# Kernel tuning notes

Measured on AMD Instinct MI355X. Metric: run time of the kernel, lower is better.

## Reference

```python
import jax, jax.numpy as jnp
import numpy as np

B_BATCH, H_DIM, W_DIM, D_MODEL, N_STATE = 4, 64, 64, 512, 8


def setup_inputs() -> dict:
    key = jax.random.key(0)
    ks = jax.random.split(key, 7)
    x = jax.random.normal(ks[0], (B_BATCH, H_DIM * W_DIM, D_MODEL), jnp.float32)
    # stable diagonal recurrence: 0 < A < 1
    A = jax.random.uniform(ks[1], (D_MODEL, N_STATE), jnp.float32, 0.5, 0.99)
    Bm = jax.random.normal(ks[2], (D_MODEL, N_STATE), jnp.float32) * 0.1
    Cm = jax.random.normal(ks[3], (D_MODEL, N_STATE), jnp.float32) * 0.1
    D_skip = jax.random.normal(ks[4], (D_MODEL,), jnp.float32)
    Wp = jax.random.normal(ks[5], (D_MODEL, D_MODEL), jnp.float32) / np.sqrt(D_MODEL)
    b_proj = jnp.zeros((D_MODEL,), jnp.float32)
    return {"x": x, "h": H_DIM, "w": W_DIM, "A": A, "Bm": Bm, "Cm": Cm,
            "D_skip": D_skip, "Wp": Wp, "b_proj": b_proj}


def _ssm(xs, A, Bm, Cm, D_skip):
    # xs: (batch', L, d). Diagonal SSM: s_t = A*s_{t-1} + B*x_t; y_t = C.s_t + D*x_t
    bt, L, d = xs.shape
    n = A.shape[1]

    def step(s, x_t):  # s: (bt, d, n), x_t: (bt, d)
        s = A * s + Bm * x_t[:, :, None]
        y = jnp.einsum('bdn,dn->bd', s, Cm) + D_skip * x_t
        return s, y

    s0 = jnp.zeros((bt, d, n), xs.dtype)
    _, ys = jax.lax.scan(step, s0, jnp.swapaxes(xs, 0, 1))  # ys: (L, bt, d)
    return jnp.swapaxes(ys, 0, 1)


def reference(x, h, w, A, Bm, Cm, D_skip, Wp, b_proj):
    b, l, d = x.shape
    xg = x.reshape(b, h, w, d)
    # horizontal direction: 'b (h w) d -> (b w) h d' -> scan over h
    x_h = jnp.transpose(xg, (0, 2, 1, 3)).reshape(b * w, h, d)
    y_h = _ssm(x_h, A, Bm, Cm, D_skip).reshape(b, w, h, d)
    y_h = jnp.transpose(y_h, (0, 2, 1, 3)).reshape(b, l, d)
    # vertical direction: 'b (h w) d -> (b h) w d' -> scan over w
    x_v = xg.reshape(b * h, w, d)
    y_v = _ssm(x_v, A, Bm, Cm, D_skip).reshape(b, l, d)
    # fused add + output projection (Linear: x @ W.T + b)
    return (y_h + y_v) @ Wp.T + b_proj
```

## Files before the change

kernel.cpp:

```cpp
#include <hip/hip_runtime.h>

#define BB 4
#define HH 64
#define WW 64
#define DD 512
#define NS 8
#define MROWS (BB * HH * WW)

typedef __attribute__((ext_vector_type(8))) __bf16 bf16x8;
typedef __attribute__((ext_vector_type(4))) float f32x4;

__device__ inline short f2bf(float f) {
  unsigned u = __float_as_uint(f);
  return (short)((u + 0x7fff + ((u >> 16) & 1)) >> 16);
}
__device__ inline float bf2f(short s) {
  return __uint_as_float(((unsigned)(unsigned short)s) << 16);
}

template <bool HORIZ>
__global__ __launch_bounds__(256) void scan_kernel(
    const float* __restrict__ x, const float* __restrict__ A,
    const float* __restrict__ Bm, const float* __restrict__ Cm,
    const float* __restrict__ Dsk, short* __restrict__ y,
    const float* __restrict__ Wp, short* __restrict__ wb) {
  if (HORIZ && blockIdx.x >= 256) {
    const int cid = (blockIdx.x - 256) * 2 + blockIdx.y;
    const int i = (cid * 256 + (int)threadIdx.x) * 8;
    const float4 v0 = *(const float4*)&Wp[i];
    const float4 v1 = *(const float4*)&Wp[i + 4];
    short r[8];
    r[0] = f2bf(v0.x); r[1] = f2bf(v0.y); r[2] = f2bf(v0.z); r[3] = f2bf(v0.w);
    r[4] = f2bf(v1.x); r[5] = f2bf(v1.y); r[6] = f2bf(v1.z); r[7] = f2bf(v1.w);
    *(short4*)&wb[i] = *(short4*)&r[0];
    *(short4*)&wb[i + 4] = *(short4*)&r[4];
    return;
  }

  const int seq = blockIdx.x;
  const int d = blockIdx.y * 256 + threadIdx.x;
  const int b = seq >> 6;
  const int r = seq & 63;

  size_t base, step;
  if (HORIZ) {
    base = ((size_t)b * HH * WW + r) * DD + d;
    step = (size_t)WW * DD;
  } else {
    base = ((size_t)(b * HH + r)) * WW * DD + d;
    step = DD;
  }

  float a[NS], bm[NS], cm[NS], s[NS];
#pragma unroll
  for (int i = 0; i < NS; i += 4) {
    float4 t;
    t = *(const float4*)&A[(size_t)d * NS + i];
    a[i] = t.x; a[i + 1] = t.y; a[i + 2] = t.z; a[i + 3] = t.w;
    t = *(const float4*)&Bm[(size_t)d * NS + i];
    bm[i] = t.x; bm[i + 1] = t.y; bm[i + 2] = t.z; bm[i + 3] = t.w;
    t = *(const float4*)&Cm[(size_t)d * NS + i];
    cm[i] = t.x; cm[i + 1] = t.y; cm[i + 2] = t.z; cm[i + 3] = t.w;
  }
  const float dk = Dsk[d];
#pragma unroll
  for (int i = 0; i < NS; ++i) s[i] = 0.f;

  float xs[2][8];
  float yp[2][8];
#pragma unroll
  for (int i = 0; i < 8; ++i) xs[0][i] = x[base + (size_t)i * step];
  if (!HORIZ) {
#pragma unroll
    for (int i = 0; i < 8; ++i) yp[0][i] = bf2f(y[base + (size_t)i * step]);
  }

#pragma unroll 2
  for (int c = 0; c < 8; ++c) {
    const int cur = c & 1, nxt = cur ^ 1;
    const size_t nbase = base + 8 * step;
    if (c < 7) {
#pragma unroll
      for (int i = 0; i < 8; ++i) xs[nxt][i] = x[nbase + (size_t)i * step];
      if (!HORIZ) {
#pragma unroll
        for (int i = 0; i < 8; ++i)
          yp[nxt][i] = bf2f(y[nbase + (size_t)i * step]);
      }
    }
#pragma unroll
    for (int i = 0; i < 8; ++i) {
      const float xv = xs[cur][i];
      float acc = dk * xv;
#pragma unroll
      for (int n = 0; n < NS; ++n) {
        s[n] = fmaf(a[n], s[n], bm[n] * xv);
        acc = fmaf(s[n], cm[n], acc);
      }
      if (!HORIZ) acc += yp[cur][i];
      y[base + (size_t)i * step] = f2bf(acc);
    }
    base = nbase;
  }
}

#define GBM 128
#define GBN 128
#define GBK 64

__global__ __launch_bounds__(256) void gemm_bf16(
    const short* __restrict__ Y, const short* __restrict__ Wb,
    const float* __restrict__ bias, float* __restrict__ out) {
  __shared__ __align__(16) short As[GBM * GBK];
  __shared__ __align__(16) short Bs[GBN * GBK];

  const int tid = threadIdx.x;
  const int lane = tid & 63;
  const int wid = tid >> 6;
  const int wm = wid >> 1, wn = wid & 1;
  const int m0 = blockIdx.y * GBM;
  const int n0 = blockIdx.x * GBN;

  const int srow = lane >> 3;
  const int scol = (lane & 7) * 8;

  f32x4 acc[4][4];
#pragma unroll
  for (int m = 0; m < 4; ++m)
#pragma unroll
    for (int n = 0; n < 4; ++n) acc[m][n] = (f32x4){0.f, 0.f, 0.f, 0.f};

  auto stage = [&](int k0) {
#pragma unroll
    for (int c = 0; c < 4; ++c) {
      const int chunk = wid * 4 + c;
      const int row = chunk * 8 + srow;
      const short* ga = &Y[(size_t)(m0 + row) * DD + k0 + scol];
      const short* gb = &Wb[(size_t)(n0 + row) * DD + k0 + scol];
      __builtin_amdgcn_global_load_lds(
          (const __attribute__((address_space(1))) unsigned int*)ga,
          (__attribute__((address_space(3))) unsigned int*)((char*)As +
                                                            chunk * 1024),
          16, 0, 0);
      __builtin_amdgcn_global_load_lds(
          (const __attribute__((address_space(1))) unsigned int*)gb,
          (__attribute__((address_space(3))) unsigned int*)((char*)Bs +
                                                            chunk * 1024),
          16, 0, 0);
    }
  };

  const int arow = wm * 64 + (lane & 15);
  const int brow = wn * 64 + (lane & 15);
  const int kfr = (lane >> 4) * 8;

  stage(0);
  const int NK = DD / GBK;
  for (int k = 0; k < NK; ++k) {
    __syncthreads();
#pragma unroll
    for (int kk = 0; kk < GBK; kk += 32) {
      bf16x8 af[4], bfr[4];
      const int kcol = kk + kfr;
#pragma unroll
      for (int m = 0; m < 4; ++m)
        af[m] = *(const bf16x8*)(const void*)&As[(arow + m * 16) * GBK + kcol];
#pragma unroll
      for (int n = 0; n < 4; ++n)
        bfr[n] = *(const bf16x8*)(const void*)&Bs[(brow + n * 16) * GBK + kcol];
#pragma unroll
      for (int m = 0; m < 4; ++m)
#pragma unroll
        for (int n = 0; n < 4; ++n)
          acc[m][n] = __builtin_amdgcn_mfma_f32_16x16x32_bf16(
              af[m], bfr[n], acc[m][n], 0, 0, 0);
    }
    if (k + 1 < NK) {
      __syncthreads();
      stage((k + 1) * GBK);
    }
  }

  const int c16 = lane & 15;
  const int r4 = (lane >> 4) * 4;
#pragma unroll
  for (int m = 0; m < 4; ++m) {
    const int rowb = m0 + wm * 64 + m * 16 + r4;
#pragma unroll
    for (int n = 0; n < 4; ++n) {
      const int col = n0 + wn * 64 + n * 16 + c16;
      const float bv = bias[col];
#pragma unroll
      for (int j = 0; j < 4; ++j)
        out[(size_t)(rowb + j) * DD + col] = acc[m][n][j] + bv;
    }
  }
}

extern "C" void kernel_launch(void* const* d_in, const int* in_sizes, int n_in,
                              void* d_out, int out_size, void* d_ws,
                              size_t ws_size, hipStream_t stream) {
  const float* x = (const float*)d_in[0];
  const float* A = (const float*)d_in[3];
  const float* Bm = (const float*)d_in[4];
  const float* Cm = (const float*)d_in[5];
  const float* Dsk = (const float*)d_in[6];
  const float* Wp = (const float*)d_in[7];
  const float* bpj = (const float*)d_in[8];
  float* out = (float*)d_out;

  short* yws = (short*)d_ws;
  short* wb = (short*)((char*)d_ws + (size_t)MROWS * DD * 2);

  const dim3 grid_h(256 + 64, DD / 256);
  scan_kernel<true><<<grid_h, 256, 0, stream>>>(x, A, Bm, Cm, Dsk, yws, Wp, wb);
  const dim3 grid_v(256, DD / 256);
  scan_kernel<false><<<grid_v, 256, 0, stream>>>(x, A, Bm, Cm, Dsk, yws, Wp,
                                                 wb);

  const dim3 gemm_grid(DD / GBN, MROWS / GBM);
  gemm_bf16<<<gemm_grid, 256, 0, stream>>>(yws, wb, bpj, out);
}
```

Before: 48.21 us.

## Fuse vertical scan with output projection GEMM in one kernel

The vertical-direction scan now runs inside the GEMM kernel. Each 512-thread block scans one image row of 64 tokens across all 512 channels and writes the summed bf16 activations straight into swizzled LDS. It then multiplies them by the full 512-column weight matrix, staged in 64-wide K slices with XOR swizzling. This removes one kernel launch and the global write and re-read of the summed activations. In exchange, each block needs 128 KB of LDS, the grid shrinks to 256 blocks, and weight staging is no longer overlapped with compute because of the extra barriers.

Measured after the change: 42.34 us. -12.2%, faster.

```diff
diff --git a/kernel.cpp b/kernel.cpp
--- a/kernel.cpp
+++ b/kernel.cpp
@@ -18,13 +18,12 @@
   return __uint_as_float(((unsigned)(unsigned short)s) << 16);
 }
 
-template <bool HORIZ>
-__global__ __launch_bounds__(256) void scan_kernel(
+__global__ __launch_bounds__(256) void scan_h_kernel(
     const float* __restrict__ x, const float* __restrict__ A,
     const float* __restrict__ Bm, const float* __restrict__ Cm,
     const float* __restrict__ Dsk, short* __restrict__ y,
     const float* __restrict__ Wp, short* __restrict__ wb) {
-  if (HORIZ && blockIdx.x >= 256) {
+  if (blockIdx.x >= 256) {
     const int cid = (blockIdx.x - 256) * 2 + blockIdx.y;
     const int i = (cid * 256 + (int)threadIdx.x) * 8;
     const float4 v0 = *(const float4*)&Wp[i];
@@ -42,14 +41,8 @@
   const int b = seq >> 6;
   const int r = seq & 63;
 
-  size_t base, step;
-  if (HORIZ) {
-    base = ((size_t)b * HH * WW + r) * DD + d;
-    step = (size_t)WW * DD;
-  } else {
-    base = ((size_t)(b * HH + r)) * WW * DD + d;
-    step = DD;
-  }
+  size_t base = ((size_t)b * HH * WW + r) * DD + d;
+  const size_t step = (size_t)WW * DD;
 
   float a[NS], bm[NS], cm[NS], s[NS];
 #pragma unroll
@@ -67,13 +60,8 @@
   for (int i = 0; i < NS; ++i) s[i] = 0.f;
 
   float xs[2][8];
-  float yp[2][8];
 #pragma unroll
   for (int i = 0; i < 8; ++i) xs[0][i] = x[base + (size_t)i * step];
-  if (!HORIZ) {
-#pragma unroll
-    for (int i = 0; i < 8; ++i) yp[0][i] = bf2f(y[base + (size_t)i * step]);
-  }
 
 #pragma unroll 2
   for (int c = 0; c < 8; ++c) {
@@ -82,11 +70,6 @@
     if (c < 7) {
 #pragma unroll
       for (int i = 0; i < 8; ++i) xs[nxt][i] = x[nbase + (size_t)i * step];
-      if (!HORIZ) {
-#pragma unroll
-        for (int i = 0; i < 8; ++i)
-          yp[nxt][i] = bf2f(y[nbase + (size_t)i * step]);
-      }
     }
 #pragma unroll
     for (int i = 0; i < 8; ++i) {
@@ -97,32 +80,93 @@
         s[n] = fmaf(a[n], s[n], bm[n] * xv);
         acc = fmaf(s[n], cm[n], acc);
       }
-      if (!HORIZ) acc += yp[cur][i];
       y[base + (size_t)i * step] = f2bf(acc);
     }
     base = nbase;
   }
 }
 
-#define GBM 128
-#define GBN 128
-#define GBK 64
-
-__global__ __launch_bounds__(256) void gemm_bf16(
-    const short* __restrict__ Y, const short* __restrict__ Wb,
-    const float* __restrict__ bias, float* __restrict__ out) {
-  __shared__ __align__(16) short As[GBM * GBK];
-  __shared__ __align__(16) short Bs[GBN * GBK];
-
-  const int tid = threadIdx.x;
+__global__ __launch_bounds__(512) void scanv_gemm_kernel(
+    const float* __restrict__ x, const float* __restrict__ A,
+    const float* __restrict__ Bm, const float* __restrict__ Cm,
+    const float* __restrict__ Dsk, const short* __restrict__ yh,
+    const short* __restrict__ Wb, const float* __restrict__ bias,
+    float* __restrict__ out) {
+  __shared__ __align__(16) short Ys[64 * DD];
+  __shared__ __align__(16) short Bs[DD * 64];
+
+  const int tid = (int)threadIdx.x;
   const int lane = tid & 63;
   const int wid = tid >> 6;
-  const int wm = wid >> 1, wn = wid & 1;
-  const int m0 = blockIdx.y * GBM;
-  const int n0 = blockIdx.x * GBN;
-
-  const int srow = lane >> 3;
-  const int scol = (lane & 7) * 8;
+  const int m0 = blockIdx.x * 64;
+  const int d = tid;
+
+  auto stageB = [&](int k0) {
+#pragma unroll
+    for (int i = 0; i < 8; ++i) {
+      const int n = i * 64 + wid * 8 + (lane >> 3);
+      const int ksw = ((lane & 7) ^ (n & 7)) << 3;
+      const short* g = &Wb[(size_t)n * DD + k0 + ksw];
+      __builtin_amdgcn_global_load_lds(
+          (const __attribute__((address_space(1))) unsigned int*)g,
+          (__attribute__((address_space(3))) unsigned int*)((char*)Bs +
+                                                            i * 8192 +
+                                                            wid * 1024),
+          16, 0, 0);
+    }
+  };
+
+  float a[NS], bm[NS], cm[NS], s[NS];
+#pragma unroll
+  for (int i = 0; i < NS; i += 4) {
+    float4 t;
+    t = *(const float4*)&A[(size_t)d * NS + i];
+    a[i] = t.x; a[i + 1] = t.y; a[i + 2] = t.z; a[i + 3] = t.w;
+    t = *(const float4*)&Bm[(size_t)d * NS + i];
+    bm[i] = t.x; bm[i + 1] = t.y; bm[i + 2] = t.z; bm[i + 3] = t.w;
+    t = *(const float4*)&Cm[(size_t)d * NS + i];
+    cm[i] = t.x; cm[i + 1] = t.y; cm[i + 2] = t.z; cm[i + 3] = t.w;
+  }
+  const float dk = Dsk[d];
+#pragma unroll
+  for (int i = 0; i < NS; ++i) s[i] = 0.f;
+
+  size_t base = (size_t)m0 * DD + d;
+  float xs[2][8], yp[2][8];
+#pragma unroll
+  for (int i = 0; i < 8; ++i) xs[0][i] = x[base + (size_t)i * DD];
+#pragma unroll
+  for (int i = 0; i < 8; ++i) yp[0][i] = bf2f(yh[base + (size_t)i * DD]);
+
+  stageB(0);
+
+#pragma unroll 2
+  for (int c = 0; c < 8; ++c) {
+    const int cur = c & 1, nxt = cur ^ 1;
+    const size_t nbase = base + 8 * DD;
+    if (c < 7) {
+#pragma unroll
+      for (int i = 0; i < 8; ++i) xs[nxt][i] = x[nbase + (size_t)i * DD];
+#pragma unroll
+      for (int i = 0; i < 8; ++i)
+        yp[nxt][i] = bf2f(yh[nbase + (size_t)i * DD]);
+    }
+#pragma unroll
+    for (int i = 0; i < 8; ++i) {
+      const int w = c * 8 + i;
+      const float xv = xs[cur][i];
+      float acc = fmaf(dk, xv, yp[cur][i]);
+#pragma unroll
+      for (int n = 0; n < NS; ++n) {
+        s[n] = fmaf(a[n], s[n], bm[n] * xv);
+        acc = fmaf(s[n], cm[n], acc);
+      }
+      Ys[w * DD + (d ^ ((w & 7) << 3))] = f2bf(acc);
+    }
+    base = nbase;
+  }
+
+  __syncthreads();
 
   f32x4 acc[4][4];
 #pragma unroll
@@ -130,54 +174,39 @@
 #pragma unroll
     for (int n = 0; n < 4; ++n) acc[m][n] = (f32x4){0.f, 0.f, 0.f, 0.f};
 
-  auto stage = [&](int k0) {
-#pragma unroll
-    for (int c = 0; c < 4; ++c) {
-      const int chunk = wid * 4 + c;
-      const int row = chunk * 8 + srow;
-      const short* ga = &Y[(size_t)(m0 + row) * DD + k0 + scol];
-      const short* gb = &Wb[(size_t)(n0 + row) * DD + k0 + scol];
-      __builtin_amdgcn_global_load_lds(
-          (const __attribute__((address_space(1))) unsigned int*)ga,
-          (__attribute__((address_space(3))) unsigned int*)((char*)As +
-                                                            chunk * 1024),
-          16, 0, 0);
-      __builtin_amdgcn_global_load_lds(
-          (const __attribute__((address_space(1))) unsigned int*)gb,
-          (__attribute__((address_space(3))) unsigned int*)((char*)Bs +
-                                                            chunk * 1024),
-          16, 0, 0);
-    }
-  };
-
-  const int arow = wm * 64 + (lane & 15);
-  const int brow = wn * 64 + (lane & 15);
+  const int fr = lane & 15;
   const int kfr = (lane >> 4) * 8;
 
-  stage(0);
-  const int NK = DD / GBK;
-  for (int k = 0; k < NK; ++k) {
-    __syncthreads();
-#pragma unroll
-    for (int kk = 0; kk < GBK; kk += 32) {
-      bf16x8 af[4], bfr[4];
-      const int kcol = kk + kfr;
-#pragma unroll
-      for (int m = 0; m < 4; ++m)
-        af[m] = *(const bf16x8*)(const void*)&As[(arow + m * 16) * GBK + kcol];
-#pragma unroll
-      for (int n = 0; n < 4; ++n)
-        bfr[n] = *(const bf16x8*)(const void*)&Bs[(brow + n * 16) * GBK + kcol];
+  for (int k = 0; k < DD / 64; ++k) {
+    const int k0 = k * 64;
+#pragma unroll
+    for (int kk = 0; kk < 64; kk += 32) {
+      bf16x8 af[4], bfv[4];
+#pragma unroll
+      for (int m = 0; m < 4; ++m) {
+        const int r = m * 16 + fr;
+        const int cc = k0 + kk + kfr;
+        af[m] = *(const bf16x8*)(const void*)&Ys[r * DD +
+                                                 (cc ^ ((r & 7) << 3))];
+      }
+#pragma unroll
+      for (int n = 0; n < 4; ++n) {
+        const int nn = wid * 64 + n * 16 + fr;
+        const int cl = kk + kfr;
+        bfv[n] = *(const bf16x8*)(const void*)&Bs[nn * 64 +
+                                                  (cl ^ ((nn & 7) << 3))];
+      }
 #pragma unroll
       for (int m = 0; m < 4; ++m)
 #pragma unroll
         for (int n = 0; n < 4; ++n)
           acc[m][n] = __builtin_amdgcn_mfma_f32_16x16x32_bf16(
-              af[m], bfr[n], acc[m][n], 0, 0, 0);
-    }
-    if (k + 1 < NK) {
+              af[m], bfv[n], acc[m][n], 0, 0, 0);
+    }
+    if (k + 1 < DD / 64) {
       __syncthreads();
-      stage((k + 1) * GBK);
+      stageB((k + 1) * 64);
+      __syncthreads();
     }
   }
 
@@ -185,10 +214,10 @@
   const int r4 = (lane >> 4) * 4;
 #pragma unroll
   for (int m = 0; m < 4; ++m) {
-    const int rowb = m0 + wm * 64 + m * 16 + r4;
+    const int rowb = m0 + m * 16 + r4;
 #pragma unroll
     for (int n = 0; n < 4; ++n) {
-      const int col = n0 + wn * 64 + n * 16 + c16;
+      const int col = wid * 64 + n * 16 + c16;
       const float bv = bias[col];
 #pragma unroll
       for (int j = 0; j < 4; ++j)
@@ -213,11 +242,8 @@
   short* wb = (short*)((char*)d_ws + (size_t)MROWS * DD * 2);
 
   const dim3 grid_h(256 + 64, DD / 256);
-  scan_kernel<true><<<grid_h, 256, 0, stream>>>(x, A, Bm, Cm, Dsk, yws, Wp, wb);
-  const dim3 grid_v(256, DD / 256);
-  scan_kernel<false><<<grid_v, 256, 0, stream>>>(x, A, Bm, Cm, Dsk, yws, Wp,
-                                                 wb);
-
-  const dim3 gemm_grid(DD / GBN, MROWS / GBM);
-  gemm_bf16<<<gemm_grid, 256, 0, stream>>>(yws, wb, bpj, out);
-}
+  scan_h_kernel<<<grid_h, 256, 0, stream>>>(x, A, Bm, Cm, Dsk, yws, Wp, wb);
+
+  scanv_gemm_kernel<<<BB * HH, 512, 0, stream>>>(x, A, Bm, Cm, Dsk, yws, wb,
+                                                 bpj, out);
+}
```

## Merge horizontal and vertical scans into one launch and concatenate-K in GEMM

Applied to the files above, without the earlier changes.

The two directional scan kernels become a single launch that writes separate bf16 buffers for the horizontal and vertical outputs. This removes the vertical pass's read-modify-write of the horizontal result and lets both directions run concurrently. The GEMM then adds the two directions by using a doubled K dimension (Yh and Yv against the same weights), and it gains a block swizzle for L2 locality plus a deeper x prefetch and a tree-reduced C dot product. In exchange the GEMM does twice the MFMA work and reads twice the A data, and the workspace grows by one activation buffer.

New measurement: 49.57 us. 1.03x slower.

```diff
diff --git a/kernel.cpp b/kernel.cpp
--- a/kernel.cpp
+++ b/kernel.cpp
@@ -14,19 +14,27 @@
   unsigned u = __float_as_uint(f);
   return (short)((u + 0x7fff + ((u >> 16) & 1)) >> 16);
 }
-__device__ inline float bf2f(short s) {
-  return __uint_as_float(((unsigned)(unsigned short)s) << 16);
-}
-
-template <bool HORIZ>
-__global__ __launch_bounds__(256) void scan_kernel(
+
+__device__ inline float ssm_step(float xv, float* s, const float* a,
+                                 const float* bm, const float* cm, float dk) {
+#pragma unroll
+  for (int n = 0; n < NS; ++n) s[n] = fmaf(a[n], s[n], bm[n] * xv);
+  float p0 = s[0] * cm[0], p1 = s[1] * cm[1], p2 = s[2] * cm[2],
+        p3 = s[3] * cm[3], p4 = s[4] * cm[4], p5 = s[5] * cm[5],
+        p6 = s[6] * cm[6], p7 = s[7] * cm[7];
+  float q0 = p0 + p1, q1 = p2 + p3, q2 = p4 + p5, q3 = p6 + p7;
+  return fmaf(dk, xv, (q0 + q1) + (q2 + q3));
+}
+
+__global__ __launch_bounds__(256) void scan_both_kernel(
     const float* __restrict__ x, const float* __restrict__ A,
     const float* __restrict__ Bm, const float* __restrict__ Cm,
-    const float* __restrict__ Dsk, short* __restrict__ y,
-    const float* __restrict__ Wp, short* __restrict__ wb) {
-  if (HORIZ && blockIdx.x >= 256) {
-    const int cid = (blockIdx.x - 256) * 2 + blockIdx.y;
-    const int i = (cid * 256 + (int)threadIdx.x) * 8;
+    const float* __restrict__ Dsk, short* __restrict__ yh,
+    short* __restrict__ yv, const float* __restrict__ Wp,
+    short* __restrict__ wb) {
+  const int bx = (int)blockIdx.x;
+  if (bx >= 1024) {
+    const int i = ((bx - 1024) * 256 + (int)threadIdx.x) * 8;
     const float4 v0 = *(const float4*)&Wp[i];
     const float4 v1 = *(const float4*)&Wp[i + 4];
     short r[8];
@@ -37,18 +45,23 @@
     return;
   }
 
-  const int seq = blockIdx.x;
-  const int d = blockIdx.y * 256 + threadIdx.x;
+  const bool horiz = (bx < 512);
+  const int lx = horiz ? bx : bx - 512;
+  const int seq = lx >> 1;
+  const int d = (lx & 1) * 256 + (int)threadIdx.x;
   const int b = seq >> 6;
   const int r = seq & 63;
 
   size_t base, step;
-  if (HORIZ) {
+  short* y;
+  if (horiz) {
     base = ((size_t)b * HH * WW + r) * DD + d;
     step = (size_t)WW * DD;
+    y = yh;
   } else {
     base = ((size_t)(b * HH + r)) * WW * DD + d;
     step = DD;
+    y = yv;
   }
 
   float a[NS], bm[NS], cm[NS], s[NS];
@@ -66,60 +79,45 @@
 #pragma unroll
   for (int i = 0; i < NS; ++i) s[i] = 0.f;
 
-  float xs[2][8];
-  float yp[2][8];
+  float xs[4][8];
 #pragma unroll
   for (int i = 0; i < 8; ++i) xs[0][i] = x[base + (size_t)i * step];
-  if (!HORIZ) {
-#pragma unroll
-    for (int i = 0; i < 8; ++i) yp[0][i] = bf2f(y[base + (size_t)i * step]);
-  }
-
-#pragma unroll 2
+#pragma unroll
+  for (int i = 0; i < 8; ++i) xs[1][i] = x[base + (size_t)(8 + i) * step];
+
+#pragma unroll 4
   for (int c = 0; c < 8; ++c) {
-    const int cur = c & 1, nxt = cur ^ 1;
-    const size_t nbase = base + 8 * step;
-    if (c < 7) {
-#pragma unroll
-      for (int i = 0; i < 8; ++i) xs[nxt][i] = x[nbase + (size_t)i * step];
-      if (!HORIZ) {
-#pragma unroll
-        for (int i = 0; i < 8; ++i)
-          yp[nxt][i] = bf2f(y[nbase + (size_t)i * step]);
-      }
-    }
-#pragma unroll
-    for (int i = 0; i < 8; ++i) {
-      const float xv = xs[cur][i];
-      float acc = dk * xv;
-#pragma unroll
-      for (int n = 0; n < NS; ++n) {
-        s[n] = fmaf(a[n], s[n], bm[n] * xv);
-        acc = fmaf(s[n], cm[n], acc);
-      }
-      if (!HORIZ) acc += yp[cur][i];
-      y[base + (size_t)i * step] = f2bf(acc);
-    }
-    base = nbase;
-  }
-}
-
-#define GBM 128
-#define GBN 128
+    const int cur = c & 3;
+    if (c < 6) {
+      const size_t pbase = base + 16 * step;
+#pragma unroll
+      for (int i = 0; i < 8; ++i)
+        xs[(c + 2) & 3][i] = x[pbase + (size_t)i * step];
+    }
+#pragma unroll
+    for (int i = 0; i < 8; ++i)
+      y[base + (size_t)i * step] = f2bf(ssm_step(xs[cur][i], s, a, bm, cm, dk));
+    base += 8 * step;
+  }
+}
+
 #define GBK 64
 
-__global__ __launch_bounds__(256) void gemm_bf16(
-    const short* __restrict__ Y, const short* __restrict__ Wb,
-    const float* __restrict__ bias, float* __restrict__ out) {
-  __shared__ __align__(16) short As[GBM * GBK];
-  __shared__ __align__(16) short Bs[GBN * GBK];
-
-  const int tid = threadIdx.x;
+__global__ __launch_bounds__(256) void gemm_cat(
+    const short* __restrict__ Yh, const short* __restrict__ Yv,
+    const short* __restrict__ Wb, const float* __restrict__ bias,
+    float* __restrict__ out) {
+  __shared__ __align__(16) short As[128 * GBK];
+  __shared__ __align__(16) short Bs[128 * GBK];
+
+  const int swz = ((int)blockIdx.x & 7) * 64 + ((int)blockIdx.x >> 3);
+  const int n0 = (swz & 3) * 128;
+  const int m0 = (swz >> 2) * 128;
+
+  const int tid = (int)threadIdx.x;
   const int lane = tid & 63;
   const int wid = tid >> 6;
   const int wm = wid >> 1, wn = wid & 1;
-  const int m0 = blockIdx.y * GBM;
-  const int n0 = blockIdx.x * GBN;
 
   const int srow = lane >> 3;
   const int scol = (lane & 7) * 8;
@@ -131,12 +129,15 @@
     for (int n = 0; n < 4; ++n) acc[m][n] = (f32x4){0.f, 0.f, 0.f, 0.f};
 
   auto stage = [&](int k0) {
+    const short* Asrc = (k0 < DD) ? Yh : Yv;
+    const int ka = k0 & (DD - 1);
+    const int kb = k0 & (DD - 1);
 #pragma unroll
     for (int c = 0; c < 4; ++c) {
       const int chunk = wid * 4 + c;
       const int row = chunk * 8 + srow;
-      const short* ga = &Y[(size_t)(m0 + row) * DD + k0 + scol];
-      const short* gb = &Wb[(size_t)(n0 + row) * DD + k0 + scol];
+      const short* ga = &Asrc[(size_t)(m0 + row) * DD + ka + scol];
+      const short* gb = &Wb[(size_t)(n0 + row) * DD + kb + scol];
       __builtin_amdgcn_global_load_lds(
           (const __attribute__((address_space(1))) unsigned int*)ga,
           (__attribute__((address_space(3))) unsigned int*)((char*)As +
@@ -155,25 +156,25 @@
   const int kfr = (lane >> 4) * 8;
 
   stage(0);
-  const int NK = DD / GBK;
+  const int NK = 2 * DD / GBK;
   for (int k = 0; k < NK; ++k) {
     __syncthreads();
 #pragma unroll
     for (int kk = 0; kk < GBK; kk += 32) {
-      bf16x8 af[4], bfr[4];
+      bf16x8 af[4], bfv[4];
       const int kcol = kk + kfr;
 #pragma unroll
       for (int m = 0; m < 4; ++m)
         af[m] = *(const bf16x8*)(const void*)&As[(arow + m * 16) * GBK + kcol];
 #pragma unroll
       for (int n = 0; n < 4; ++n)
-        bfr[n] = *(const bf16x8*)(const void*)&Bs[(brow + n * 16) * GBK + kcol];
+        bfv[n] = *(const bf16x8*)(const void*)&Bs[(brow + n * 16) * GBK + kcol];
 #pragma unroll
       for (int m = 0; m < 4; ++m)
 #pragma unroll
         for (int n = 0; n < 4; ++n)
           acc[m][n] = __builtin_amdgcn_mfma_f32_16x16x32_bf16(
-              af[m], bfr[n], acc[m][n], 0, 0, 0);
+              af[m], bfv[n], acc[m][n], 0, 0, 0);
     }
     if (k + 1 < NK) {
       __syncthreads();
@@ -209,15 +210,11 @@
   const float* bpj = (const float*)d_in[8];
   float* out = (float*)d_out;
 
-  short* yws = (short*)d_ws;
-  short* wb = (short*)((char*)d_ws + (size_t)MROWS * DD * 2);
-
-  const dim3 grid_h(256 + 64, DD / 256);
-  scan_kernel<true><<<grid_h, 256, 0, stream>>>(x, A, Bm, Cm, Dsk, yws, Wp, wb);
-  const dim3 grid_v(256, DD / 256);
-  scan_kernel<false><<<grid_v, 256, 0, stream>>>(x, A, Bm, Cm, Dsk, yws, Wp,
-                                                 wb);
-
-  const dim3 gemm_grid(DD / GBN, MROWS / GBM);
-  gemm_bf16<<<gemm_grid, 256, 0, stream>>>(yws, wb, bpj, out);
-}
+  short* yh = (short*)d_ws;
+  short* yv = yh + (size_t)MROWS * DD;
+  short* wb = yv + (size_t)MROWS * DD;
+
+  scan_both_kernel<<<1152, 256, 0, stream>>>(x, A, Bm, Cm, Dsk, yh, yv, Wp, wb);
+
+  gemm_cat<<<512, 256, 0, stream>>>(yh, yv, wb, bpj, out);
+}
```
